# Performance work log

Hardware: AMD Instinct MI355X
Metric: run time of the kernel (lower is better)

Reference implementation:

```python
import jax, jax.numpy as jnp
import numpy as np

H = 4
N = 50000
D_IN = 128
D_MODEL = 256
NCLASS = 40
B_S = 1
BH = B_S * H
LN_EPS = 1e-5


def sparse_perm_1D(indices, values, feats, n, bh):
    """Batched sparse (bh,n,n) @ dense (bh,n,d): gather -> scale -> segment-sum scatter."""
    gathered = feats[indices[0], indices[2]]              # (nnz, d)
    contrib = values[:, None] * gathered                   # (nnz, d)
    seg = indices[0] * n + indices[1]                      # (nnz,)
    out = jax.ops.segment_sum(contrib, seg, num_segments=bh * n)
    return out.reshape(bh, n, -1)


def layer_norm(x, gamma, beta):
    mu = jnp.mean(x, axis=-1, keepdims=True)
    var = jnp.var(x, axis=-1, keepdims=True)
    return (x - mu) * jax.lax.rsqrt(var + LN_EPS) * gamma + beta


def setup_inputs() -> dict:
    key = jax.random.key(0)
    k1, k2, k3, k4, k5, k6, k7 = jax.random.split(key, 7)
    # per-(batch*head) permutation sigma: nonzero at (b, i, sigma_b(i))
    perm_keys = jax.random.split(k1, BH)
    sigma = jax.vmap(lambda k: jax.random.permutation(k, N))(perm_keys)  # (BH, N)
    b_idx = jnp.repeat(jnp.arange(BH), N)
    row_idx = jnp.tile(jnp.arange(N), BH)
    col_idx = sigma.reshape(-1)
    perm_indices = jnp.stack([b_idx, row_idx, col_idx], axis=0).astype(jnp.int32)  # (3, BH*N)
    perm_values = jax.random.uniform(k2, (BH * N,), dtype=jnp.float32)
    features = jax.random.normal(k3, (B_S, N, D_IN), dtype=jnp.float32)
    appd = jax.random.normal(k4, (B_S, N, D_IN), dtype=jnp.float32)
    # parameters
    w_scale_in = 1.0 / np.sqrt(2 * D_IN)
    W_in = jax.random.uniform(k5, (2 * D_IN, D_MODEL), dtype=jnp.float32, minval=-w_scale_in, maxval=w_scale_in)
    b_in = jnp.zeros((D_MODEL,), dtype=jnp.float32)
    ln_gamma = jnp.ones((D_MODEL * H,), dtype=jnp.float32)
    ln_beta = jnp.zeros((D_MODEL * H,), dtype=jnp.float32)
    w_scale_h = 1.0 / np.sqrt(D_MODEL * H)
    W_head = jax.random.uniform(k6, (D_MODEL * H, NCLASS), dtype=jnp.float32, minval=-w_scale_h, maxval=w_scale_h)
    b_head = jax.random.uniform(k7, (NCLASS,), dtype=jnp.float32, minval=-w_scale_h, maxval=w_scale_h)
    return {"perm_indices": perm_indices, "perm_values": perm_values,
            "features": features, "appd": appd,
            "W_in": W_in, "b_in": b_in,
            "ln_gamma": ln_gamma, "ln_beta": ln_beta,
            "W_head": W_head, "b_head": b_head}


def reference(perm_indices, perm_values, features, appd, W_in, b_in, ln_gamma, ln_beta, W_head, b_head):
    # concat auxiliary features, replicate per head: (B_S,N,2*D_IN) -> (BH,N,2*D_IN)
    feat = jnp.concatenate([features, appd], axis=-1)
    feat = jnp.broadcast_to(feat[:, None], (B_S, H, N, 2 * D_IN)).reshape(BH, N, 2 * D_IN)
    # permute rows: perm @ feat
    x = sparse_perm_1D(perm_indices, perm_values, feat, N, BH)
    # ff_in + relu (dropout is identity at eval)
    x = jax.nn.relu(x @ W_in + b_in)                       # (BH, N, D_MODEL)
    # nlayers == nblocks == 0: compress/uncompress loops are empty
    # inverse permutation: perm^T @ x (swap row/col indices)
    idx_t = jnp.stack([perm_indices[0], perm_indices[2], perm_indices[1]], axis=0)
    y = sparse_perm_1D(idx_t, perm_values, x, N, BH)       # (BH, N, D_MODEL)
    # (B_S,H,N,D) -> (B_S,N,H*D)
    y = y.reshape(B_S, H, N, D_MODEL).transpose(0, 2, 1, 3).reshape(B_S, N, H * D_MODEL)
    y = layer_norm(y, ln_gamma, ln_beta)
    return y @ W_head + b_head                             # (B_S, N, NCLASS)
```

## Files before the change

kernel.cpp:

```cpp
#include <hip/hip_runtime.h>

#define NROW 50000
#define DIN 128
#define DM 256
#define HH 4
#define NC 40
#define BHN 200000
#define NBLK 782

typedef float f32x4 __attribute__((ext_vector_type(4)));
typedef short bf16x8 __attribute__((ext_vector_type(8)));

__device__ __forceinline__ unsigned short f2bf(float x) {
    unsigned int u = __float_as_uint(x);
    u += 0x7fffu + ((u >> 16) & 1u);
    return (unsigned short)(u >> 16);
}

__global__ __launch_bounds__(256) void k_scatter(const int* __restrict__ pi,
                                                 const float* __restrict__ pv,
                                                 float* __restrict__ vcol) {
    int k = blockIdx.x * 256 + threadIdx.x;
    if (k < BHN) {
        int b   = pi[k];
        int col = pi[2 * BHN + k];
        vcol[b * NROW + col] = pv[k];
    }
}

__global__ __launch_bounds__(256) void k_prep_wt(const float* __restrict__ Win,
                                                 unsigned short* __restrict__ Wt) {
    int n = blockIdx.x, k = threadIdx.x;
    Wt[n * DM + k] = f2bf(Win[k * DM + n]);
}

__global__ __launch_bounds__(256) void k_prep_wh(const float* __restrict__ Wh,
                                                 const float* __restrict__ gamma,
                                                 const float* __restrict__ beta,
                                                 const float* __restrict__ bh,
                                                 unsigned short* __restrict__ Wgt,
                                                 float* __restrict__ bias2) {
    __shared__ float red[256];
    int c = blockIdx.x, tid = threadIdx.x;
    float part = 0.f;
    #pragma unroll
    for (int q = 0; q < 4; ++q) {
        int d = tid + 256 * q;
        float w = Wh[d * NC + c];
        Wgt[c * 1024 + d] = f2bf(gamma[d] * w);
        part = fmaf(beta[d], w, part);
    }
    red[tid] = part;
    __syncthreads();
    for (int s = 128; s > 0; s >>= 1) {
        if (tid < s) red[tid] += red[tid + s];
        __syncthreads();
    }
    if (tid == 0) bias2[c] = bh[c] + red[0];
}

__global__ __launch_bounds__(256, 2) void k_fused(
    const float* __restrict__ feats, const float* __restrict__ appd,
    const unsigned short* __restrict__ Wt,
    const unsigned short* __restrict__ Wgt,
    const float* __restrict__ vcol,
    const float* __restrict__ b_in,
    const float* __restrict__ bias2,
    float* __restrict__ out)
{
    __shared__ __align__(16) unsigned short Abuf[64 * 264];
    __shared__ __align__(16) unsigned short Wbuf[48 * 264];
    __shared__ float vsL[HH][64];
    __shared__ float binL[DM];
    __shared__ float b2L[48];

    const int tid = threadIdx.x;
    const int wv = tid >> 6;
    const int ln = tid & 63;
    const int quad = ln >> 4;
    const int lr = ln & 15;
    const int j0 = blockIdx.x * 64;

    #pragma unroll
    for (int q = 0; q < 16; ++q) {
        int cid = tid + 256 * q;
        int r = cid >> 6;
        int k4 = (cid & 63) << 2;
        int jr = j0 + r;
        float4 v = make_float4(0.f, 0.f, 0.f, 0.f);
        if (jr < NROW)
            v = (k4 < DIN) ? *(const float4*)&feats[(size_t)jr * DIN + k4]
                           : *(const float4*)&appd[(size_t)jr * DIN + k4 - DIN];
        ushort4 b;
        b.x = f2bf(v.x); b.y = f2bf(v.y); b.z = f2bf(v.z); b.w = f2bf(v.w);
        *(ushort4*)&Abuf[r * 264 + k4] = b;
    }
    if (tid < 64) {
        int j = min(j0 + tid, NROW - 1);
        #pragma unroll
        for (int h = 0; h < HH; ++h) vsL[h][tid] = vcol[h * NROW + j];
    }
    binL[tid] = b_in[tid];
    if (tid < 48) b2L[tid] = (tid < NC) ? bias2[tid] : 0.f;
    __syncthreads();

    const f32x4 zero4 = {0.f, 0.f, 0.f, 0.f};
    f32x4 accG[16];
    #pragma unroll
    for (int t = 0; t < 16; ++t) accG[t] = zero4;

    for (int kc = 0; kc < 8; ++kc) {
        {
            const unsigned short* src = Wt + tid * DM + kc * 32;
            unsigned short* dst = &Wbuf[tid * 40];
            #pragma unroll
            for (int jq = 0; jq < 4; ++jq) {
                uint4 w4 = *(const uint4*)(src + jq * 8);
                *(uint4*)(dst + jq * 8) = w4;
            }
        }
        __syncthreads();
        bf16x8 af = *(const bf16x8*)&Abuf[(wv * 16 + lr) * 264 + kc * 32 + quad * 8];
        #pragma unroll
        for (int t = 0; t < 16; ++t) {
            bf16x8 bf = *(const bf16x8*)&Wbuf[(t * 16 + lr) * 40 + quad * 8];
            accG[t] = __builtin_amdgcn_mfma_f32_16x16x32_bf16(af, bf, accG[t], 0, 0, 0);
        }
        __syncthreads();
    }

    float vh_r[HH][4];
    #pragma unroll
    for (int h = 0; h < HH; ++h)
        #pragma unroll
        for (int rg = 0; rg < 4; ++rg)
            vh_r[h][rg] = vsL[h][wv * 16 + quad * 4 + rg];
    float bcol[16];
    #pragma unroll
    for (int t = 0; t < 16; ++t) bcol[t] = binL[t * 16 + lr];

    float s[4] = {0.f, 0.f, 0.f, 0.f}, q2[4] = {0.f, 0.f, 0.f, 0.f};
    #pragma unroll
    for (int t = 0; t < 16; ++t)
        #pragma unroll
        for (int rg = 0; rg < 4; ++rg) {
            float gg = accG[t][rg];
            #pragma unroll
            for (int h = 0; h < HH; ++h) {
                float v = vh_r[h][rg];
                float y = v * fmaxf(fmaf(v, gg, bcol[t]), 0.f);
                s[rg] += y;
                q2[rg] = fmaf(y, y, q2[rg]);
            }
        }
    #pragma unroll
    for (int m = 1; m <= 8; m <<= 1)
        #pragma unroll
        for (int rg = 0; rg < 4; ++rg) {
            s[rg] += __shfl_xor(s[rg], m);
            q2[rg] += __shfl_xor(q2[rg], m);
        }
    float mu_[4], rs_[4];
    #pragma unroll
    for (int rg = 0; rg < 4; ++rg) {
        float m = s[rg] * (1.f / 1024.f);
        float var = q2[rg] * (1.f / 1024.f) - m * m;
        mu_[rg] = m;
        rs_[rg] = rsqrtf(var + 1e-5f);
    }

    f32x4 accO[3];
    #pragma unroll
    for (int t = 0; t < 3; ++t) accO[t] = zero4;

    for (int h = 0; h < HH; ++h) {
        __syncthreads();
        #pragma unroll
        for (int t = 0; t < 16; ++t)
            #pragma unroll
            for (int rg = 0; rg < 4; ++rg) {
                float v = vh_r[h][rg];
                float y = v * fmaxf(fmaf(v, accG[t][rg], bcol[t]), 0.f);
                float z = (y - mu_[rg]) * rs_[rg];
                Abuf[(wv * 16 + quad * 4 + rg) * 264 + t * 16 + lr] = f2bf(z);
            }
        #pragma unroll
        for (int q = 0; q < 6; ++q) {
            int e = tid + 256 * q;
            int c = e >> 5;
            int dd = (e & 31) << 3;
            uint4 w4 = make_uint4(0u, 0u, 0u, 0u);
            if (c < NC) w4 = *(const uint4*)&Wgt[c * 1024 + h * DM + dd];
            *(uint4*)&Wbuf[c * 264 + dd] = w4;
        }
        __syncthreads();
        #pragma unroll
        for (int kc = 0; kc < 8; ++kc) {
            bf16x8 af = *(const bf16x8*)&Abuf[(wv * 16 + lr) * 264 + kc * 32 + quad * 8];
            #pragma unroll
            for (int t = 0; t < 3; ++t) {
                bf16x8 bf = *(const bf16x8*)&Wbuf[(t * 16 + lr) * 264 + kc * 32 + quad * 8];
                accO[t] = __builtin_amdgcn_mfma_f32_16x16x32_bf16(af, bf, accO[t], 0, 0, 0);
            }
        }
    }

    #pragma unroll
    for (int t = 0; t < 3; ++t)
        #pragma unroll
        for (int rg = 0; rg < 4; ++rg) {
            int row = j0 + wv * 16 + quad * 4 + rg;
            int c = t * 16 + lr;
            if (row < NROW && c < NC)
                out[(size_t)row * NC + c] = accO[t][rg] + b2L[c];
        }
}

extern "C" void kernel_launch(void* const* d_in, const int* in_sizes, int n_in,
                              void* d_out, int out_size, void* d_ws, size_t ws_size,
                              hipStream_t stream) {
    const int*   pi    = (const int*)d_in[0];
    const float* pv    = (const float*)d_in[1];
    const float* feats = (const float*)d_in[2];
    const float* appd  = (const float*)d_in[3];
    const float* Win   = (const float*)d_in[4];
    const float* b_in  = (const float*)d_in[5];
    const float* gamma = (const float*)d_in[6];
    const float* beta  = (const float*)d_in[7];
    const float* Wh    = (const float*)d_in[8];
    const float* bh    = (const float*)d_in[9];
    float* out = (float*)d_out;

    char* w = (char*)d_ws;
    float*          vcolW  = (float*)w;
    float*          bias2W = (float*)(w + 800000);
    unsigned short* WtW    = (unsigned short*)(w + 800192);
    unsigned short* WgtW   = (unsigned short*)(w + 931264);

    k_scatter<<<(BHN + 255) / 256, 256, 0, stream>>>(pi, pv, vcolW);
    k_prep_wt<<<DM, 256, 0, stream>>>(Win, WtW);
    k_prep_wh<<<NC, 256, 0, stream>>>(Wh, gamma, beta, bh, WgtW, bias2W);
    k_fused<<<NBLK, 256, 0, stream>>>(feats, appd, WtW, WgtW, vcolW, b_in, bias2W, out);
}
```

Baseline: 168.7 us.

## Merge prep kernels and split first GEMM by output columns per wave

The three prep kernels (scatter, W_in transpose, head-weight fold) become one launch that dispatches on block index. In the fused kernel each wave now computes all 64 rows for its own 64-column slice of the first GEMM. A-operands are loaded straight from global memory and B-operands read from the prepared weights in global/L2, so the LDS staging buffers and most barriers go away. LayerNorm statistics are reduced across waves through a small shared buffer. The head GEMM reads its weights directly from global memory, trading LDS traffic for repeated L2 reads and more registers.

```diff
diff --git a/kernel.cpp b/kernel.cpp
--- a/kernel.cpp
+++ b/kernel.cpp
@@ -1,4 +1,5 @@
 #include <hip/hip_runtime.h>
+#include <hip/hip_bf16.h>
 
 #define NROW 50000
 #define DIN 128
@@ -17,62 +18,67 @@
     return (unsigned short)(u >> 16);
 }
 
-__global__ __launch_bounds__(256) void k_scatter(const int* __restrict__ pi,
-                                                 const float* __restrict__ pv,
-                                                 float* __restrict__ vcol) {
-    int k = blockIdx.x * 256 + threadIdx.x;
-    if (k < BHN) {
-        int b   = pi[k];
-        int col = pi[2 * BHN + k];
-        vcol[b * NROW + col] = pv[k];
-    }
-}
-
-__global__ __launch_bounds__(256) void k_prep_wt(const float* __restrict__ Win,
-                                                 unsigned short* __restrict__ Wt) {
-    int n = blockIdx.x, k = threadIdx.x;
-    Wt[n * DM + k] = f2bf(Win[k * DM + n]);
-}
-
-__global__ __launch_bounds__(256) void k_prep_wh(const float* __restrict__ Wh,
-                                                 const float* __restrict__ gamma,
-                                                 const float* __restrict__ beta,
-                                                 const float* __restrict__ bh,
-                                                 unsigned short* __restrict__ Wgt,
-                                                 float* __restrict__ bias2) {
-    __shared__ float red[256];
-    int c = blockIdx.x, tid = threadIdx.x;
-    float part = 0.f;
-    #pragma unroll
-    for (int q = 0; q < 4; ++q) {
-        int d = tid + 256 * q;
-        float w = Wh[d * NC + c];
-        Wgt[c * 1024 + d] = f2bf(gamma[d] * w);
-        part = fmaf(beta[d], w, part);
-    }
-    red[tid] = part;
-    __syncthreads();
-    for (int s = 128; s > 0; s >>= 1) {
-        if (tid < s) red[tid] += red[tid + s];
-        __syncthreads();
-    }
-    if (tid == 0) bias2[c] = bh[c] + red[0];
+__device__ __forceinline__ unsigned int pk2(float lo, float hi) {
+    __hip_bfloat162 h = __float22bfloat162_rn(make_float2(lo, hi));
+    return *(unsigned int*)&h;
+}
+
+__global__ __launch_bounds__(256) void k_prep(const int* __restrict__ pi,
+                                              const float* __restrict__ pv,
+                                              const float* __restrict__ Win,
+                                              const float* __restrict__ Wh,
+                                              const float* __restrict__ gamma,
+                                              const float* __restrict__ beta,
+                                              const float* __restrict__ bh,
+                                              float* __restrict__ vcol,
+                                              unsigned short* __restrict__ Wt,
+                                              unsigned short* __restrict__ Wgtp,
+                                              float* __restrict__ bias2) {
+    const int bid = blockIdx.x, tid = threadIdx.x;
+    if (bid < 782) {
+        int k = bid * 256 + tid;
+        if (k < BHN) {
+            int b   = pi[k];
+            int col = pi[2 * BHN + k];
+            vcol[b * NROW + col] = pv[k];
+        }
+    } else if (bid == 782) {
+        #pragma unroll 4
+        for (int q = 0; q < 192; ++q) {
+            int e = q * 256 + tid;
+            int c = e >> 10, d = e & 1023;
+            Wgtp[c * 1024 + d] = (c < NC) ? f2bf(gamma[d] * Wh[d * NC + c]) : (unsigned short)0;
+        }
+    } else if (bid == 783) {
+        if (tid < NC) {
+            float a = bh[tid];
+            #pragma unroll 8
+            for (int d = 0; d < 1024; ++d) a = fmaf(beta[d], Wh[d * NC + tid], a);
+            bias2[tid] = a;
+        }
+    } else {
+        int base = (bid - 784) * 4096;
+        #pragma unroll 4
+        for (int q = 0; q < 16; ++q) {
+            int e = base + q * 256 + tid;
+            int n = e >> 8, k = e & 255;
+            Wt[n * DM + k] = f2bf(Win[k * DM + n]);
+        }
+    }
 }
 
 __global__ __launch_bounds__(256, 2) void k_fused(
     const float* __restrict__ feats, const float* __restrict__ appd,
     const unsigned short* __restrict__ Wt,
-    const unsigned short* __restrict__ Wgt,
+    const unsigned short* __restrict__ Wgtp,
     const float* __restrict__ vcol,
     const float* __restrict__ b_in,
     const float* __restrict__ bias2,
     float* __restrict__ out)
 {
-    __shared__ __align__(16) unsigned short Abuf[64 * 264];
-    __shared__ __align__(16) unsigned short Wbuf[48 * 264];
+    __shared__ __align__(16) unsigned short zbuf[4][64 * 72];
+    __shared__ float sred[2][64][4];
     __shared__ float vsL[HH][64];
-    __shared__ float binL[DM];
-    __shared__ float b2L[48];
 
     const int tid = threadIdx.x;
     const int wv = tid >> 6;
@@ -80,126 +86,139 @@
     const int quad = ln >> 4;
     const int lr = ln & 15;
     const int j0 = blockIdx.x * 64;
-
-    #pragma unroll
-    for (int q = 0; q < 16; ++q) {
-        int cid = tid + 256 * q;
-        int r = cid >> 6;
-        int k4 = (cid & 63) << 2;
-        int jr = j0 + r;
-        float4 v = make_float4(0.f, 0.f, 0.f, 0.f);
-        if (jr < NROW)
-            v = (k4 < DIN) ? *(const float4*)&feats[(size_t)jr * DIN + k4]
-                           : *(const float4*)&appd[(size_t)jr * DIN + k4 - DIN];
-        ushort4 b;
-        b.x = f2bf(v.x); b.y = f2bf(v.y); b.z = f2bf(v.z); b.w = f2bf(v.w);
-        *(ushort4*)&Abuf[r * 264 + k4] = b;
-    }
+    const int colbase = wv * 64;
+
     if (tid < 64) {
         int j = min(j0 + tid, NROW - 1);
         #pragma unroll
         for (int h = 0; h < HH; ++h) vsL[h][tid] = vcol[h * NROW + j];
     }
-    binL[tid] = b_in[tid];
-    if (tid < 48) b2L[tid] = (tid < NC) ? bias2[tid] : 0.f;
     __syncthreads();
 
+    float bt[4];
+    #pragma unroll
+    for (int t = 0; t < 4; ++t) bt[t] = b_in[colbase + t * 16 + lr];
+    float b2[3];
+    #pragma unroll
+    for (int t = 0; t < 3; ++t) {
+        int c = t * 16 + lr;
+        b2[t] = (c < NC) ? bias2[c] : 0.f;
+    }
+
+    int ar[4];
+    #pragma unroll
+    for (int rt = 0; rt < 4; ++rt) ar[rt] = min(j0 + rt * 16 + lr, NROW - 1);
+
     const f32x4 zero4 = {0.f, 0.f, 0.f, 0.f};
-    f32x4 accG[16];
-    #pragma unroll
-    for (int t = 0; t < 16; ++t) accG[t] = zero4;
+    f32x4 accG[4][4];
+    #pragma unroll
+    for (int rt = 0; rt < 4; ++rt)
+        #pragma unroll
+        for (int t = 0; t < 4; ++t) accG[rt][t] = zero4;
 
     for (int kc = 0; kc < 8; ++kc) {
-        {
-            const unsigned short* src = Wt + tid * DM + kc * 32;
-            unsigned short* dst = &Wbuf[tid * 40];
-            #pragma unroll
-            for (int jq = 0; jq < 4; ++jq) {
-                uint4 w4 = *(const uint4*)(src + jq * 8);
-                *(uint4*)(dst + jq * 8) = w4;
-            }
-        }
+        const float* src = (kc < 4) ? feats : appd;
+        const int ko = (kc & 3) * 32 + quad * 8;
+        bf16x8 af[4];
+        #pragma unroll
+        for (int rt = 0; rt < 4; ++rt) {
+            float4 x0 = *(const float4*)&src[(size_t)ar[rt] * DIN + ko];
+            float4 x1 = *(const float4*)&src[(size_t)ar[rt] * DIN + ko + 4];
+            union { unsigned int ui[4]; bf16x8 v; } u;
+            u.ui[0] = pk2(x0.x, x0.y);
+            u.ui[1] = pk2(x0.z, x0.w);
+            u.ui[2] = pk2(x1.x, x1.y);
+            u.ui[3] = pk2(x1.z, x1.w);
+            af[rt] = u.v;
+        }
+        #pragma unroll
+        for (int t = 0; t < 4; ++t) {
+            bf16x8 bf = *(const bf16x8*)&Wt[(size_t)(colbase + t * 16 + lr) * DM + kc * 32 + quad * 8];
+            #pragma unroll
+            for (int rt = 0; rt < 4; ++rt)
+                accG[rt][t] = __builtin_amdgcn_mfma_f32_16x16x32_bf16(af[rt], bf, accG[rt][t], 0, 0, 0);
+        }
+    }
+
+    float s[4][4] = {}, ss[4][4] = {};
+    for (int h = 0; h < HH; ++h) {
+        #pragma unroll
+        for (int rt = 0; rt < 4; ++rt)
+            #pragma unroll
+            for (int rg = 0; rg < 4; ++rg) {
+                float v = vsL[h][rt * 16 + quad * 4 + rg];
+                #pragma unroll
+                for (int t = 0; t < 4; ++t) {
+                    float y = v * fmaxf(fmaf(v, accG[rt][t][rg], bt[t]), 0.f);
+                    s[rt][rg] += y;
+                    ss[rt][rg] = fmaf(y, y, ss[rt][rg]);
+                }
+            }
+    }
+    #pragma unroll
+    for (int m = 1; m <= 8; m <<= 1)
+        #pragma unroll
+        for (int rt = 0; rt < 4; ++rt)
+            #pragma unroll
+            for (int rg = 0; rg < 4; ++rg) {
+                s[rt][rg] += __shfl_xor(s[rt][rg], m);
+                ss[rt][rg] += __shfl_xor(ss[rt][rg], m);
+            }
+    if (lr == 0) {
+        #pragma unroll
+        for (int rt = 0; rt < 4; ++rt)
+            #pragma unroll
+            for (int rg = 0; rg < 4; ++rg) {
+                int r = rt * 16 + quad * 4 + rg;
+                sred[0][r][wv] = s[rt][rg];
+                sred[1][r][wv] = ss[rt][rg];
+            }
+    }
+    __syncthreads();
+    float rs[4][4], nm[4][4];
+    #pragma unroll
+    for (int rt = 0; rt < 4; ++rt)
+        #pragma unroll
+        for (int rg = 0; rg < 4; ++rg) {
+            int r = rt * 16 + quad * 4 + rg;
+            f32x4 s4 = *(const f32x4*)&sred[0][r][0];
+            f32x4 q4 = *(const f32x4*)&sred[1][r][0];
+            float S = (s4.x + s4.y) + (s4.z + s4.w);
+            float Q = (q4.x + q4.y) + (q4.z + q4.w);
+            float mm = S * (1.f / 1024.f);
+            float var = Q * (1.f / 1024.f) - mm * mm;
+            float r_ = rsqrtf(var + 1e-5f);
+            rs[rt][rg] = r_;
+            nm[rt][rg] = -mm * r_;
+        }
+
+    f32x4 accO[3];
+    #pragma unroll
+    for (int t = 0; t < 3; ++t) accO[t] = zero4;
+    unsigned short* zb = zbuf[wv];
+
+    for (int h = 0; h < HH; ++h) {
+        if (h) __syncthreads();
+        #pragma unroll
+        for (int rt = 0; rt < 4; ++rt)
+            #pragma unroll
+            for (int rg = 0; rg < 4; ++rg) {
+                float v = vsL[h][rt * 16 + quad * 4 + rg];
+                float r_ = rs[rt][rg], n_ = nm[rt][rg];
+                #pragma unroll
+                for (int t = 0; t < 4; ++t) {
+                    float y = v * fmaxf(fmaf(v, accG[rt][t][rg], bt[t]), 0.f);
+                    float z = fmaf(y, r_, n_);
+                    zb[(rt * 16 + quad * 4 + rg) * 72 + t * 16 + lr] = f2bf(z);
+                }
+            }
         __syncthreads();
-        bf16x8 af = *(const bf16x8*)&Abuf[(wv * 16 + lr) * 264 + kc * 32 + quad * 8];
-        #pragma unroll
-        for (int t = 0; t < 16; ++t) {
-            bf16x8 bf = *(const bf16x8*)&Wbuf[(t * 16 + lr) * 40 + quad * 8];
-            accG[t] = __builtin_amdgcn_mfma_f32_16x16x32_bf16(af, bf, accG[t], 0, 0, 0);
-        }
-        __syncthreads();
-    }
-
-    float vh_r[HH][4];
-    #pragma unroll
-    for (int h = 0; h < HH; ++h)
-        #pragma unroll
-        for (int rg = 0; rg < 4; ++rg)
-            vh_r[h][rg] = vsL[h][wv * 16 + quad * 4 + rg];
-    float bcol[16];
-    #pragma unroll
-    for (int t = 0; t < 16; ++t) bcol[t] = binL[t * 16 + lr];
-
-    float s[4] = {0.f, 0.f, 0.f, 0.f}, q2[4] = {0.f, 0.f, 0.f, 0.f};
-    #pragma unroll
-    for (int t = 0; t < 16; ++t)
-        #pragma unroll
-        for (int rg = 0; rg < 4; ++rg) {
-            float gg = accG[t][rg];
-            #pragma unroll
-            for (int h = 0; h < HH; ++h) {
-                float v = vh_r[h][rg];
-                float y = v * fmaxf(fmaf(v, gg, bcol[t]), 0.f);
-                s[rg] += y;
-                q2[rg] = fmaf(y, y, q2[rg]);
-            }
-        }
-    #pragma unroll
-    for (int m = 1; m <= 8; m <<= 1)
-        #pragma unroll
-        for (int rg = 0; rg < 4; ++rg) {
-            s[rg] += __shfl_xor(s[rg], m);
-            q2[rg] += __shfl_xor(q2[rg], m);
-        }
-    float mu_[4], rs_[4];
-    #pragma unroll
-    for (int rg = 0; rg < 4; ++rg) {
-        float m = s[rg] * (1.f / 1024.f);
-        float var = q2[rg] * (1.f / 1024.f) - m * m;
-        mu_[rg] = m;
-        rs_[rg] = rsqrtf(var + 1e-5f);
-    }
-
-    f32x4 accO[3];
-    #pragma unroll
-    for (int t = 0; t < 3; ++t) accO[t] = zero4;
-
-    for (int h = 0; h < HH; ++h) {
-        __syncthreads();
-        #pragma unroll
-        for (int t = 0; t < 16; ++t)
-            #pragma unroll
-            for (int rg = 0; rg < 4; ++rg) {
-                float v = vh_r[h][rg];
-                float y = v * fmaxf(fmaf(v, accG[t][rg], bcol[t]), 0.f);
-                float z = (y - mu_[rg]) * rs_[rg];
-                Abuf[(wv * 16 + quad * 4 + rg) * 264 + t * 16 + lr] = f2bf(z);
-            }
-        #pragma unroll
-        for (int q = 0; q < 6; ++q) {
-            int e = tid + 256 * q;
-            int c = e >> 5;
-            int dd = (e & 31) << 3;
-            uint4 w4 = make_uint4(0u, 0u, 0u, 0u);
-            if (c < NC) w4 = *(const uint4*)&Wgt[c * 1024 + h * DM + dd];
-            *(uint4*)&Wbuf[c * 264 + dd] = w4;
-        }
-        __syncthreads();
         #pragma unroll
         for (int kc = 0; kc < 8; ++kc) {
-            bf16x8 af = *(const bf16x8*)&Abuf[(wv * 16 + lr) * 264 + kc * 32 + quad * 8];
+            bf16x8 af = *(const bf16x8*)&zbuf[kc >> 1][(wv * 16 + lr) * 72 + (kc & 1) * 32 + quad * 8];
             #pragma unroll
             for (int t = 0; t < 3; ++t) {
-                bf16x8 bf = *(const bf16x8*)&Wbuf[(t * 16 + lr) * 264 + kc * 32 + quad * 8];
+                bf16x8 bf = *(const bf16x8*)&Wgtp[(size_t)(t * 16 + lr) * 1024 + h * 256 + kc * 32 + quad * 8];
                 accO[t] = __builtin_amdgcn_mfma_f32_16x16x32_bf16(af, bf, accO[t], 0, 0, 0);
             }
         }
@@ -212,7 +231,7 @@
             int row = j0 + wv * 16 + quad * 4 + rg;
             int c = t * 16 + lr;
             if (row < NROW && c < NC)
-                out[(size_t)row * NC + c] = accO[t][rg] + b2L[c];
+                out[(size_t)row * NC + c] = accO[t][rg] + b2[t];
         }
 }
 
@@ -233,12 +252,10 @@
 
     char* w = (char*)d_ws;
     float*          vcolW  = (float*)w;
-    float*          bias2W = (float*)(w + 800000);
-    unsigned short* WtW    = (unsigned short*)(w + 800192);
-    unsigned short* WgtW   = (unsigned short*)(w + 931264);
-
-    k_scatter<<<(BHN + 255) / 256, 256, 0, stream>>>(pi, pv, vcolW);
-    k_prep_wt<<<DM, 256, 0, stream>>>(Win, WtW);
-    k_prep_wh<<<NC, 256, 0, stream>>>(Wh, gamma, beta, bh, WgtW, bias2W);
-    k_fused<<<NBLK, 256, 0, stream>>>(feats, appd, WtW, WgtW, vcolW, b_in, bias2W, out);
-}
+    unsigned short* WtW    = (unsigned short*)(w + 800000);
+    unsigned short* WgtpW  = (unsigned short*)(w + 931072);
+    float*          bias2W = (float*)(w + 1029376);
+
+    k_prep<<<800, 256, 0, stream>>>(pi, pv, Win, Wh, gamma, beta, bh, vcolW, WtW, WgtpW, bias2W);
+    k_fused<<<NBLK, 256, 0, stream>>>(feats, appd, WtW, WgtpW, vcolW, b_in, bias2W, out);
+}
```

New measurement: 233.6 us. 1.39x slower.
